# Optimization experiments

Hardware: AMD Instinct MI355X
Metric: run time of the kernel (lower is better)

## Reference

```python
import jax, jax.numpy as jnp
import numpy as np

B, N, RD = 32, 2000, 32
E, H, A = 128, 256, 8
NUM_ACTIONS = N
ACTION_NORM = float(NUM_ACTIONS)


def _mlp2(x, W1, b1, W2, b2):
    return jnp.maximum(x @ W1 + b1, 0.0) @ W2 + b2


def setup_inputs() -> dict:
    key = jax.random.key(0)
    ks = jax.random.split(key, 8)
    s = lambda fan_in: 1.0 / np.sqrt(fan_in)
    return {
        "state": jax.random.normal(ks[0], (B, N, RD), jnp.float32),
        "distance_matrix": jax.random.uniform(ks[1], (N, N), jnp.float32),
        "W_emb1": jax.random.normal(ks[2], (RD, H), jnp.float32) * s(RD),
        "b_emb1": jnp.zeros((H,), jnp.float32),
        "W_emb2": jax.random.normal(ks[3], (H, E), jnp.float32) * s(H),
        "b_emb2": jnp.zeros((E,), jnp.float32),
        "Wq1": jax.random.normal(ks[4], (E + A, H), jnp.float32) * s(E + A),
        "bq1": jnp.zeros((H,), jnp.float32),
        "Wq2": jax.random.normal(ks[5], (H, 1), jnp.float32) * s(H),
        "bq2": jnp.zeros((1,), jnp.float32),
        "fixed_actions": jax.random.randint(ks[6], (3, B), 0, NUM_ACTIONS, jnp.int32),
        "fixed_agent_ids": jnp.arange(3, dtype=jnp.int32),
    }


def reference(state, distance_matrix, W_emb1, b_emb1, W_emb2, b_emb2,
              Wq1, bq1, Wq2, bq2, fixed_actions, fixed_agent_ids):
    # normalized distance -> similarity, row-stochastic
    dm = distance_matrix / distance_matrix.max()
    sim = jnp.exp(-dm)  # scaling = 1 (use_nn_scaling=False)
    sim = sim / sim.sum(-1, keepdims=True)

    enc = _mlp2(state, W_emb1, b_emb1, W_emb2, b_emb2)      # [B,N,E]
    x = jnp.einsum('nm,bme->bne', sim, enc)                 # graph conv mix

    idx_f = jnp.arange(N, dtype=x.dtype)

    def qnet(actions):
        # actions: [B,A] broadcast over node axis -> concat -> MLP -> [B,N]
        act = jnp.broadcast_to(actions[:, None, :], (B, N, A))
        feat = jnp.concatenate([x, act], axis=-1)           # [B,N,E+A]
        return _mlp2(feat, Wq1, bq1, Wq2, bq2)[..., 0]      # [B,N]

    # init actions: -1 everywhere, fixed agents get given action / norm
    actions = jnp.full((B, A), -1.0, dtype=x.dtype)
    actions = actions.at[:, fixed_agent_ids].set(
        fixed_actions.T.astype(x.dtype) / ACTION_NORM)

    # sequential per-agent soft-argmax loop (second torch loop; the first
    # torch loop's q-values are fully overwritten here, so it is dead code)
    q_cols = []
    for agent_id in range(A):
        q = qnet(actions)                                   # [B,N]
        sam = jnp.clip(jax.nn.softmax(q, axis=-1) @ idx_f, 0.0, float(NUM_ACTIONS))
        actions = actions.at[:, agent_id].set(
            jax.lax.stop_gradient(sam / ACTION_NORM))
        q2 = qnet(actions)
        qv = jnp.take_along_axis(q2, sam.astype(jnp.int32)[:, None], axis=-1)[:, 0]
        q_cols.append(qv)

    q_values = jnp.stack(q_cols, axis=1)                    # [B,A]
    chosen = (actions * ACTION_NORM).astype(jnp.int32)      # [B,A]
    return q_values, chosen
```

## Files before the change

kernel.cpp:

```cpp
#include <hip/hip_runtime.h>
#include <cstddef>

#define NB 32
#define NN 2000
#define NRD 32
#define NE 128
#define NH 256
#define NA 8
#define KP8 2048
#define NGP 128
#define H1S 264
#define XT8S 136
#define ACTION_NORM 2000.0f

typedef unsigned short u16;
typedef unsigned char u8;
typedef __bf16 b16x8 __attribute__((ext_vector_type(8)));
typedef float f32x4 __attribute__((ext_vector_type(4)));
typedef const __attribute__((address_space(1))) unsigned int* gptr_t;
typedef __attribute__((address_space(3))) unsigned int* lptr_t;

__device__ inline u16 f2bf(float x) {
    unsigned u = __float_as_uint(x);
    u += 0x7FFFu + ((u >> 16) & 1u);
    return (u16)(u >> 16);
}
__device__ inline float bf2f(u16 h) { return __uint_as_float((unsigned)h << 16); }
__device__ inline u8 f2fp8(float x) {
    return (u8)(__builtin_amdgcn_cvt_pk_fp8_f32(x, x, 0, false) & 0xFF);
}
__device__ inline u16 f2fp8x2(float a, float b) {
    return (u16)(__builtin_amdgcn_cvt_pk_fp8_f32(a, b, 0, false) & 0xFFFF);
}
__device__ inline float fp82f(u8 b) {
    return __builtin_amdgcn_cvt_pk_f32_fp8((unsigned)b, false)[0];
}
__device__ inline int kswz(int m) {
    return (m & ~63) + (((m >> 3) & 3) << 4) + (((m >> 5) & 1) << 3) + (m & 7);
}

#define PREP_STATE (64000 * 32)
#define PREP_W1T   (256 * 32)
#define PREP_W2T   (128 * 256)
#define PREP_WQ1T  (256 * 128)
#define PREP_PAD   (4096 * 48)
#define PREP_TOT   (PREP_STATE + PREP_W1T + PREP_W2T + PREP_WQ1T + PREP_PAD)
#define PREP_BLOCKS (PREP_TOT / 256)
#define MAX_BLOCKS 1024
__global__ __launch_bounds__(256) void k_front(
        const float* __restrict__ state, const float* __restrict__ W1,
        const float* __restrict__ W2, const float* __restrict__ Wq1,
        const float* __restrict__ dm, const int* __restrict__ fa,
        const int* __restrict__ fid,
        u16* __restrict__ state_b, u16* __restrict__ W1t,
        u16* __restrict__ W2t, u8* __restrict__ Wq1f8,
        u8* __restrict__ encb, float* __restrict__ pmax,
        float* __restrict__ actions, float* __restrict__ ap0,
        float2* __restrict__ part0) {
    __shared__ float sh[256];
    const int blk = blockIdx.x, t = threadIdx.x;
    if (blk < PREP_BLOCKS) {
        int i = blk * 256 + t;
        if (i < PREP_STATE) { state_b[i] = f2bf(state[i]); return; }
        i -= PREP_STATE;
        if (i < PREP_W1T) { int h = i >> 5, k = i & 31; W1t[i] = f2bf(W1[k * NH + h]); return; }
        i -= PREP_W1T;
        if (i < PREP_W2T) { int e = i >> 8, h = i & 255; W2t[i] = f2bf(W2[h * NE + e]); return; }
        i -= PREP_W2T;
        if (i < PREP_WQ1T) { int hq = i >> 7, e = i & 127; Wq1f8[i] = f2fp8(Wq1[e * NH + hq]); return; }
        i -= PREP_WQ1T;
        if (i < PREP_PAD) { int eb = i / 48, mm = NN + (i % 48); encb[(size_t)eb * KP8 + kswz(mm)] = 0; }
        return;
    }
    if (blk < PREP_BLOCKS + MAX_BLOCKS) {
        const int bid = blk - PREP_BLOCKS;
        float m = 0.0f;
        for (size_t i = (size_t)bid * 256 + t; i < (size_t)NN * NN; i += (size_t)MAX_BLOCKS * 256)
            m = fmaxf(m, dm[i]);
        sh[t] = m; __syncthreads();
        for (int s = 128; s > 0; s >>= 1) {
            if (t < s) sh[t] = fmaxf(sh[t], sh[t + s]);
            __syncthreads();
        }
        if (t == 0) pmax[bid] = sh[0];
        return;
    }
    const int b = t >> 3, a = t & 7;
    float v = -1.0f;
    for (int j = 0; j < 3; ++j)
        if (fid[j] == a) v = (float)fa[j * NB + b] / ACTION_NORM;
    actions[t] = v;
    sh[t] = v;
    __syncthreads();
    float wq[NA];
#pragma unroll
    for (int aa = 0; aa < NA; ++aa) wq[aa] = Wq1[(size_t)(NE + aa) * NH + t];
    for (int bb = 0; bb < NB; ++bb) {
        float s = 0.0f;
#pragma unroll
        for (int aa = 0; aa < NA; ++aa) s = fmaf(sh[bb * NA + aa], wq[aa], s);
        ap0[bb * NH + t] = s;
    }
    for (int i = t; i < NB * NGP; i += 256) part0[i] = make_float2(0.0f, 0.0f);
}

__global__ __launch_bounds__(512) void k_sim_enc(
        const u16* __restrict__ state_b, const u16* __restrict__ W1t,
        const u16* __restrict__ W2t, u8* __restrict__ encb,
        const float* __restrict__ b1, const float* __restrict__ b2,
        const float* __restrict__ dm, const float* __restrict__ pmax,
        u8* __restrict__ simb, float* __restrict__ inv_rs) {
    __shared__ u16 stage[20 * 512];
    __shared__ u16 h1t[64 * H1S];
    const int blk = blockIdx.x, tid = threadIdx.x;

    if (blk >= 1000) {
        float* shf = (float*)stage;
        const int n = blk - 1000, t = tid;
        float m = fmaxf(pmax[t], pmax[t + 512]);
        shf[t] = m; __syncthreads();
        for (int s = 256; s > 0; s >>= 1) {
            if (t < s) shf[t] = fmaxf(shf[t], shf[t + s]);
            __syncthreads();
        }
        const float inv = 1.0f / shf[0];
        __syncthreads();
        float s = 0.0f;
        for (int mm = t * 2; mm < KP8; mm += 1024) {
            float e0 = 0.0f, e1 = 0.0f;
            if (mm < NN)     { e0 = expf(-dm[(size_t)n * NN + mm] * inv);     s += e0; }
            if (mm + 1 < NN) { e1 = expf(-dm[(size_t)n * NN + mm + 1] * inv); s += e1; }
            *(u16*)(simb + (size_t)n * KP8 + kswz(mm)) = f2fp8x2(e0, e1);
        }
        shf[t] = s; __syncthreads();
        for (int st = 256; st > 0; st >>= 1) {
            if (t < st) shf[t] += shf[t + st];
            __syncthreads();
        }
        if (t == 0) inv_rs[n] = 1.0f / shf[0];
        return;
    }

    const int w = tid >> 6, l = tid & 63;
    const int lm = l & 15, lq = l >> 4;
    const int gm = blk * 64;

    {
#pragma unroll
        for (int i = 0; i < 3; ++i) {
            const int idx = w * 3 + i;
            if (idx < 20) {
                const u16* gp;
                if (idx < 4) gp = state_b + (size_t)(gm + idx * 16 + lm) * NRD + lq * 8;
                else         gp = W1t + (size_t)((idx - 4) * 16 + lm) * NRD + lq * 8;
                __builtin_amdgcn_global_load_lds((gptr_t)gp, (lptr_t)(stage + idx * 512), 16, 0, 0);
            }
        }
        __syncthreads();
        b16x8 af[4], bf[2];
#pragma unroll
        for (int i = 0; i < 4; ++i) af[i] = *(const b16x8*)(stage + i * 512 + l * 8);
#pragma unroll
        for (int j = 0; j < 2; ++j) bf[j] = *(const b16x8*)(stage + (4 + w * 2 + j) * 512 + l * 8);
        f32x4 acc1[4][2] = {};
#pragma unroll
        for (int i = 0; i < 4; ++i)
#pragma unroll
            for (int j = 0; j < 2; ++j)
                acc1[i][j] = __builtin_amdgcn_mfma_f32_16x16x32_bf16(af[i], bf[j], acc1[i][j], 0, 0, 0);
#pragma unroll
        for (int i = 0; i < 4; ++i)
#pragma unroll
            for (int r = 0; r < 4; ++r) {
                const int row = i * 16 + lq * 4 + r;
#pragma unroll
                for (int j = 0; j < 2; ++j) {
                    const int col = w * 32 + j * 16 + lm;
                    h1t[row * H1S + col] = f2bf(fmaxf(acc1[i][j][r] + b1[col], 0.0f));
                }
            }
    }

    const int wr = w & 3, wc = w >> 2;
    f32x4 acc2[2][2] = {};
    const u16* gpw = W2t + (size_t)(w * 16 + lm) * NH + lq * 8;
    __syncthreads();
    __builtin_amdgcn_global_load_lds((gptr_t)gpw, (lptr_t)(stage + w * 512), 16, 0, 0);
    __syncthreads();
    for (int t = 0; t < 8; ++t) {
        const int cur = t & 1;
        if (t < 7) {
            gpw += 32;
            __builtin_amdgcn_global_load_lds((gptr_t)gpw,
                (lptr_t)(stage + (cur ^ 1) * 4096 + w * 512), 16, 0, 0);
        }
        const u16* base = stage + cur * 4096;
        b16x8 af2[2], bf2[2];
#pragma unroll
        for (int i = 0; i < 2; ++i)
            af2[i] = *(const b16x8*)(base + (wr * 2 + i) * 512 + l * 8);
#pragma unroll
        for (int j = 0; j < 2; ++j)
            bf2[j] = *(const b16x8*)(h1t + (wc * 32 + j * 16 + lm) * H1S + t * 32 + lq * 8);
#pragma unroll
        for (int i = 0; i < 2; ++i)
#pragma unroll
            for (int j = 0; j < 2; ++j)
                acc2[i][j] = __builtin_amdgcn_mfma_f32_16x16x32_bf16(af2[i], bf2[j], acc2[i][j], 0, 0, 0);
        __syncthreads();
    }
#pragma unroll
    for (int i = 0; i < 2; ++i)
#pragma unroll
        for (int r = 0; r < 4; ++r) {
            const int e = wr * 32 + i * 16 + lq * 4 + r;
            const float bias = b2[e];
#pragma unroll
            for (int j = 0; j < 2; ++j) {
                const int rg = gm + wc * 32 + j * 16 + lm;
                const unsigned bb = (unsigned)rg / 2000u;
                const unsigned mm = (unsigned)rg - bb * 2000u;
                encb[((size_t)bb * 128 + e) * KP8 + kswz((int)mm)] = f2fp8(acc2[i][j][r] + bias);
            }
        }
}

__global__ __launch_bounds__(512) void k_conv_y0(
        const u8* __restrict__ simb, const u8* __restrict__ encb,
        const u8* __restrict__ Wq1f8, const float* __restrict__ inv_rs,
        const float* __restrict__ bq1, const float* __restrict__ ap0,
        const float* __restrict__ Wq2, u8* __restrict__ y0f8,
        float2* __restrict__ part0) {
    __shared__ u8 lds[3 * 16384];
    __shared__ float qsum[64 * 8];
    const int tid = threadIdx.x;
    const int w = tid >> 6, l = tid & 63;
    const int wr = w & 1, wc = w >> 1;
    const int bm = blockIdx.x * 128;
    const int bb = blockIdx.y;
    const int lm = l & 15, lq = l >> 4;
    const u8* Bt = encb + (size_t)bb * 128 * KP8;
    typedef long lx2 __attribute__((ext_vector_type(2)));

    f32x4 acc[4][2] = {};

    const u8* gpt[2];
#pragma unroll
    for (int i = 0; i < 2; ++i) {
        const int idx = w * 2 + i;
        if (idx < 8) {
            int row = bm + idx * 16 + lm;
            row = row < NN ? row : NN - 1;
            gpt[i] = simb + (size_t)row * KP8 + lq * 16;
        } else {
            gpt[i] = Bt + (size_t)((idx - 8) * 16 + lm) * KP8 + lq * 16;
        }
    }

    auto STAGE = [&](int kt, int buf) {
#pragma unroll
        for (int i = 0; i < 2; ++i)
            __builtin_amdgcn_global_load_lds((gptr_t)(gpt[i] + kt * 64),
                (lptr_t)(lds + buf * 16384 + (w * 2 + i) * 1024), 16, 0, 0);
    };
    auto COMPUTE = [&](int buf) {
        const u8* curb = lds + buf * 16384;
        const int fo = l * 16;
        lx2 af[4], bf[2];
#pragma unroll
        for (int i = 0; i < 4; ++i)
            af[i] = *(const lx2*)(curb + (wr * 4 + i) * 1024 + fo);
#pragma unroll
        for (int j = 0; j < 2; ++j)
            bf[j] = *(const lx2*)(curb + (8 + wc * 2 + j) * 1024 + fo);
        __builtin_amdgcn_s_setprio(1);
#pragma unroll
        for (int i = 0; i < 4; ++i)
#pragma unroll
            for (int j = 0; j < 2; ++j) {
                acc[i][j] = __builtin_amdgcn_mfma_f32_16x16x32_fp8_fp8(af[i][0], bf[j][0], acc[i][j], 0, 0, 0);
                acc[i][j] = __builtin_amdgcn_mfma_f32_16x16x32_fp8_fp8(af[i][1], bf[j][1], acc[i][j], 0, 0, 0);
            }
        __builtin_amdgcn_s_setprio(0);
    };

#define FENCE() __builtin_amdgcn_sched_barrier(0)
#define BAR_BARE() do { FENCE(); asm volatile("" ::: "memory"); \
    __builtin_amdgcn_s_barrier(); FENCE(); } while (0)
#define BAR_VM(N) do { FENCE(); asm volatile("s_waitcnt vmcnt(" #N ")" ::: "memory"); \
    __builtin_amdgcn_s_barrier(); FENCE(); } while (0)

    STAGE(0, 0);
    STAGE(1, 1);
    for (int t = 0; t < 30; ++t) {
        STAGE(t + 2, (t + 2) % 3);
        BAR_VM(4);
        COMPUTE(t % 3);
        BAR_BARE();
    }
    BAR_VM(2);
    COMPUTE(0);
    BAR_BARE();
    BAR_VM(0);
    COMPUTE(1);
    BAR_BARE();
#undef BAR_VM
#undef BAR_BARE
#undef FENCE

#pragma unroll
    for (int i = 0; i < 4; ++i) {
#pragma unroll
        for (int r = 0; r < 4; ++r) {
            const int row = wr * 64 + i * 16 + lq * 4 + r;
            const int gn = bm + row;
            const float rsv = inv_rs[gn < NN ? gn : NN - 1];
#pragma unroll
            for (int j = 0; j < 2; ++j) {
                const int col = wc * 32 + j * 16 + lm;
                lds[row * XT8S + col] = f2fp8(acc[i][j][r] * rsv);
            }
        }
    }
    __syncthreads();

    const int h0 = w * 32;
    float bq1v[2], apv[2], w2vv[2];
#pragma unroll
    for (int j = 0; j < 2; ++j) {
        const int h = h0 + j * 16 + lm;
        bq1v[j] = bq1[h];
        apv[j] = ap0[bb * NH + h];
        w2vv[j] = Wq2[h];
    }
    float se_tot = 0.0f, sn_tot = 0.0f;

    for (int half = 0; half < 2; ++half) {
        f32x4 acc2[4][2] = {};
#pragma unroll
        for (int ks = 0; ks < 4; ++ks) {
            long bfw[2];
#pragma unroll
            for (int j = 0; j < 2; ++j)
                bfw[j] = *(const long*)(Wq1f8 + (size_t)(h0 + j * 16 + lm) * NE + ks * 32 + lq * 8);
#pragma unroll
            for (int i = 0; i < 4; ++i) {
                const long afx = *(const long*)(lds + (half * 64 + i * 16 + lm) * XT8S + ks * 32 + lq * 8);
#pragma unroll
                for (int j = 0; j < 2; ++j)
                    acc2[i][j] = __builtin_amdgcn_mfma_f32_16x16x32_fp8_fp8(afx, bfw[j], acc2[i][j], 0, 0, 0);
            }
        }
#pragma unroll
        for (int i = 0; i < 4; ++i) {
#pragma unroll
            for (int r = 0; r < 4; ++r) {
                const int rl = i * 16 + lq * 4 + r;
                const int n = bm + half * 64 + rl;
                float q = 0.0f;
#pragma unroll
                for (int j = 0; j < 2; ++j) {
                    const float v = acc2[i][j][r] + bq1v[j];
                    if (n < NN) y0f8[((size_t)n * NB + bb) * NH + h0 + j * 16 + lm] = f2fp8(v);
                    q += fmaxf(v + apv[j], 0.0f) * w2vv[j];
                }
#pragma unroll
                for (int off = 1; off < 16; off <<= 1) q += __shfl_xor(q, off);
                if (lm == 0) qsum[rl * 8 + w] = q;
            }
        }
        __syncthreads();
        if (tid < 64) {
            const int n = bm + half * 64 + tid;
            float q = 0.0f;
#pragma unroll
            for (int wv = 0; wv < 8; ++wv) q += qsum[tid * 8 + wv];
            float e = (n < NN) ? expf(fminf(q, 60.0f)) : 0.0f;
            float sne = e * (float)n;
#pragma unroll
            for (int off = 32; off > 0; off >>= 1) {
                e += __shfl_xor(e, off); sne += __shfl_xor(sne, off);
            }
            if (tid == 0) { se_tot += e; sn_tot += sne; }
        }
        __syncthreads();
    }
    if (tid == 0) part0[bb * NGP + blockIdx.x] = make_float2(se_tot, sn_tot);
}

__global__ __launch_bounds__(256) void k_agent(
        const u8* __restrict__ y0f8, const float* __restrict__ Wq1,
        const float* __restrict__ Wq2, const float* __restrict__ bq2,
        float* actions, const float2* __restrict__ pin, float2* __restrict__ pout,
        float* __restrict__ out, int ag) {
    __shared__ float sh[256];
    __shared__ float s_sam;
    const int t = threadIdx.x;
    const int lane = t & 63, wave = t >> 6;
    const int wg = blockIdx.x * 4 + wave;
    const int b = wg & 31, ng = wg >> 5;
    const int hl = lane & 15, qtr = lane >> 4;

    float act[NA];
#pragma unroll
    for (int a = 0; a < NA; ++a) act[a] = actions[b * NA + a];
    {
        const float2 p0 = pin[b * NGP + lane];
        const float2 p1 = pin[b * NGP + 64 + lane];
        float se0 = p0.x + p1.x, sn0 = p0.y + p1.y;
#pragma unroll
        for (int m = 32; m > 0; m >>= 1) {
            se0 += __shfl_xor(se0, m); sn0 += __shfl_xor(sn0, m);
        }
        const float sam = fminf(fmaxf(sn0 / se0, 0.0f), 2000.0f);
        act[ag - 1] = sam * (1.0f / ACTION_NORM);
    }
    float ap16[16] = {};
#pragma unroll
    for (int a = 0; a < NA; ++a) {
        const float av = act[a];
        const float4* wq = (const float4*)(Wq1 + (size_t)(NE + a) * NH + hl * 16);
#pragma unroll
        for (int jj = 0; jj < 4; ++jj) {
            const float4 w4 = wq[jj];
            ap16[jj * 4 + 0] = fmaf(av, w4.x, ap16[jj * 4 + 0]);
            ap16[jj * 4 + 1] = fmaf(av, w4.y, ap16[jj * 4 + 1]);
            ap16[jj * 4 + 2] = fmaf(av, w4.z, ap16[jj * 4 + 2]);
            ap16[jj * 4 + 3] = fmaf(av, w4.w, ap16[jj * 4 + 3]);
        }
    }
    float w2v[16];
    {
        const float4* w2p = (const float4*)(Wq2 + hl * 16);
#pragma unroll
        for (int jj = 0; jj < 4; ++jj) {
            const float4 w4 = w2p[jj];
            w2v[jj * 4 + 0] = w4.x; w2v[jj * 4 + 1] = w4.y;
            w2v[jj * 4 + 2] = w4.z; w2v[jj * 4 + 3] = w4.w;
        }
    }

    float se = 0.0f, sn = 0.0f;
#pragma unroll
    for (int k = 0; k < 4; ++k) {
        const int p = ng + k * NGP;
        if (p >= NN / 4) break;
        const int n = 4 * p + qtr;
        const uint4 yv = *(const uint4*)(y0f8 + (((size_t)n * NB + b) << 8) + hl * 16);
        const unsigned dw[4] = {yv.x, yv.y, yv.z, yv.w};
        float q = 0.0f;
#pragma unroll
        for (int d = 0; d < 4; ++d) {
            const auto lo = __builtin_amdgcn_cvt_pk_f32_fp8(dw[d], false);
            const auto hi = __builtin_amdgcn_cvt_pk_f32_fp8(dw[d], true);
            q += fmaxf(lo[0] + ap16[d * 4 + 0], 0.f) * w2v[d * 4 + 0];
            q += fmaxf(lo[1] + ap16[d * 4 + 1], 0.f) * w2v[d * 4 + 1];
            q += fmaxf(hi[0] + ap16[d * 4 + 2], 0.f) * w2v[d * 4 + 2];
            q += fmaxf(hi[1] + ap16[d * 4 + 3], 0.f) * w2v[d * 4 + 3];
        }
#pragma unroll
        for (int off = 1; off < 16; off <<= 1) q += __shfl_xor(q, off);
        const float e = expf(fminf(q, 60.0f));
        se += e; sn += e * (float)n;
    }
    se += __shfl_xor(se, 16); sn += __shfl_xor(sn, 16);
    se += __shfl_xor(se, 32); sn += __shfl_xor(sn, 32);
    if (lane == 0) pout[b * NGP + ng] = make_float2(se, sn);

    if (blockIdx.x < NB) {
        const int bb = blockIdx.x;
        if (wave == 0) {
            const float2 p0 = pin[bb * NGP + lane];
            const float2 p1 = pin[bb * NGP + 64 + lane];
            float a1 = p0.x + p1.x, a2 = p0.y + p1.y;
#pragma unroll
            for (int m = 32; m > 0; m >>= 1) {
                a1 += __shfl_xor(a1, m); a2 += __shfl_xor(a2, m);
            }
            if (lane == 0) s_sam = fminf(fmaxf(a2 / a1, 0.0f), 2000.0f);
        }
        __syncthreads();
        const float sam = s_sam;
        const float samn = sam * (1.0f / ACTION_NORM);
        float apt = 0.0f;
#pragma unroll
        for (int a = 0; a < NA; ++a) {
            const float av = (a == ag - 1) ? samn : actions[bb * NA + a];
            apt = fmaf(av, Wq1[(size_t)(NE + a) * NH + t], apt);
        }
        int nsel = (int)sam; if (nsel > NN - 1) nsel = NN - 1;
        const float yv = fp82f(y0f8[((size_t)nsel * NB + bb) * NH + t]);
        sh[t] = fmaxf(yv + apt, 0.0f) * Wq2[t];
        __syncthreads();
        for (int s = 128; s > 0; s >>= 1) {
            if (t < s) sh[t] += sh[t + s];
            __syncthreads();
        }
        if (t == 0) {
            out[bb * NA + (ag - 1)] = sh[0] + bq2[0];
            actions[bb * NA + (ag - 1)] = samn;
        }
    }
}

__global__ __launch_bounds__(256) void k_fin(
        const u8* __restrict__ y0f8, const float* __restrict__ Wq1,
        const float* __restrict__ Wq2, const float* __restrict__ bq2,
        const float* __restrict__ actions, const float2* __restrict__ pin,
        float* __restrict__ out) {
    __shared__ float sh[256];
    __shared__ float s_sam;
    const int bb = blockIdx.x, t = threadIdx.x;
    const int lane = t & 63, wave = t >> 6;
    if (wave == 0) {
        const float2 p0 = pin[bb * NGP + lane];
        const float2 p1 = pin[bb * NGP + 64 + lane];
        float a1 = p0.x + p1.x, a2 = p0.y + p1.y;
#pragma unroll
        for (int m = 32; m > 0; m >>= 1) {
            a1 += __shfl_xor(a1, m); a2 += __shfl_xor(a2, m);
        }
        if (lane == 0) s_sam = fminf(fmaxf(a2 / a1, 0.0f), 2000.0f);
    }
    __syncthreads();
    const float sam = s_sam;
    const float samn = sam * (1.0f / ACTION_NORM);
    float apt = 0.0f;
#pragma unroll
    for (int a = 0; a < NA; ++a) {
        const float av = (a == NA - 1) ? samn : actions[bb * NA + a];
        apt = fmaf(av, Wq1[(size_t)(NE + a) * NH + t], apt);
    }
    int nsel = (int)sam; if (nsel > NN - 1) nsel = NN - 1;
    const float yv = fp82f(y0f8[((size_t)nsel * NB + bb) * NH + t]);
    sh[t] = fmaxf(yv + apt, 0.0f) * Wq2[t];
    __syncthreads();
    for (int s = 128; s > 0; s >>= 1) {
        if (t < s) sh[t] += sh[t + s];
        __syncthreads();
    }
    if (t == 0) out[bb * NA + (NA - 1)] = sh[0] + bq2[0];
    if (t < NA) {
        const float av = (t == NA - 1) ? samn : actions[bb * NA + t];
        out[NB * NA + bb * NA + t] = (float)(int)(av * ACTION_NORM);
    }
}

extern "C" void kernel_launch(void* const* d_in, const int* in_sizes, int n_in,
                              void* d_out, int out_size, void* d_ws, size_t ws_size,
                              hipStream_t stream) {
    const float* state = (const float*)d_in[0];
    const float* dm    = (const float*)d_in[1];
    const float* W1    = (const float*)d_in[2];
    const float* b1    = (const float*)d_in[3];
    const float* W2    = (const float*)d_in[4];
    const float* b2    = (const float*)d_in[5];
    const float* Wq1   = (const float*)d_in[6];
    const float* bq1   = (const float*)d_in[7];
    const float* Wq2   = (const float*)d_in[8];
    const float* bq2   = (const float*)d_in[9];
    const int* fa      = (const int*)d_in[10];
    const int* fid     = (const int*)d_in[11];
    float* out = (float*)d_out;

    char* p = (char*)d_ws;
    u8* simb       = (u8*)p;       p += (size_t)NN * KP8;
    u8* encb       = (u8*)p;       p += (size_t)4096 * KP8;
    float* inv_rs  = (float*)p;    p += 2048 * 4;
    float* pmax    = (float*)p;    p += 1024 * 4;
    float* actions = (float*)p;    p += 256 * 4;
    float* ap0     = (float*)p;    p += 8192 * 4;
    float2* part0  = (float2*)p;   p += (size_t)NB * NGP * 8;
    float2* part1  = (float2*)p;   p += (size_t)NB * NGP * 8;
    u16* state_b   = (u16*)p;      p += (size_t)2048000 * 2;
    u16* W1t       = (u16*)p;      p += 8192 * 2;
    u16* W2t       = (u16*)p;      p += 32768 * 2;
    u8* Wq1f8      = (u8*)p;       p += 32768;
    u8* y0f8       = (u8*)p;       p += (size_t)16384000;

    k_front<<<PREP_BLOCKS + MAX_BLOCKS + 1, 256, 0, stream>>>(
        state, W1, W2, Wq1, dm, fa, fid,
        state_b, W1t, W2t, Wq1f8, encb, pmax, actions, ap0, part0);
    k_sim_enc<<<3000, 512, 0, stream>>>(state_b, W1t, W2t, encb, b1, b2,
                                        dm, pmax, simb, inv_rs);
    k_conv_y0<<<dim3(16, 32), 512, 0, stream>>>(simb, encb, Wq1f8, inv_rs, bq1,
                                                ap0, Wq2, y0f8, part0);
    for (int ag = 1; ag < NA; ++ag) {
        const float2* pin  = (ag & 1) ? part0 : part1;
        float2*       pout = (ag & 1) ? part1 : part0;
        k_agent<<<1024, 256, 0, stream>>>(y0f8, Wq1, Wq2, bq2, actions,
                                          pin, pout, out, ag);
    }
    k_fin<<<NB, 256, 0, stream>>>(y0f8, Wq1, Wq2, bq2, actions, part1, out);
}
```

Baseline: 260.0 us.

## Fuse sequential agent loop into one persistent per-batch kernel; deepen conv LDS ring

```diff
diff --git a/kernel.cpp b/kernel.cpp
--- a/kernel.cpp
+++ b/kernel.cpp
@@ -231,7 +231,7 @@
         const float* __restrict__ bq1, const float* __restrict__ ap0,
         const float* __restrict__ Wq2, u8* __restrict__ y0f8,
         float2* __restrict__ part0) {
-    __shared__ u8 lds[3 * 16384];
+    __shared__ u8 lds[4 * 16384];
     __shared__ float qsum[64 * 8];
     const int tid = threadIdx.x;
     const int w = tid >> 6, l = tid & 63;
@@ -285,27 +285,21 @@
     };
 
 #define FENCE() __builtin_amdgcn_sched_barrier(0)
-#define BAR_BARE() do { FENCE(); asm volatile("" ::: "memory"); \
-    __builtin_amdgcn_s_barrier(); FENCE(); } while (0)
 #define BAR_VM(N) do { FENCE(); asm volatile("s_waitcnt vmcnt(" #N ")" ::: "memory"); \
     __builtin_amdgcn_s_barrier(); FENCE(); } while (0)
 
     STAGE(0, 0);
     STAGE(1, 1);
     for (int t = 0; t < 30; ++t) {
-        STAGE(t + 2, (t + 2) % 3);
+        STAGE(t + 2, (t + 2) & 3);
         BAR_VM(4);
-        COMPUTE(t % 3);
-        BAR_BARE();
+        COMPUTE(t & 3);
     }
     BAR_VM(2);
-    COMPUTE(0);
-    BAR_BARE();
+    COMPUTE(2);
     BAR_VM(0);
-    COMPUTE(1);
-    BAR_BARE();
+    COMPUTE(3);
 #undef BAR_VM
-#undef BAR_BARE
 #undef FENCE
 
 #pragma unroll
@@ -388,161 +382,130 @@
     if (tid == 0) part0[bb * NGP + blockIdx.x] = make_float2(se_tot, sn_tot);
 }
 
-__global__ __launch_bounds__(256) void k_agent(
+__global__ __launch_bounds__(1024) void k_agents7(
         const u8* __restrict__ y0f8, const float* __restrict__ Wq1,
         const float* __restrict__ Wq2, const float* __restrict__ bq2,
-        float* actions, const float2* __restrict__ pin, float2* __restrict__ pout,
-        float* __restrict__ out, int ag) {
-    __shared__ float sh[256];
-    __shared__ float s_sam;
+        const float* __restrict__ actions, const float* __restrict__ ap0,
+        const float2* __restrict__ part0, float* __restrict__ out) {
+    __shared__ float s_w1r[NA][NH];
+    __shared__ float s_w2[NH];
+    __shared__ float2 s_part[16];
+    __shared__ float s_red[256];
+    const int b = blockIdx.x;
     const int t = threadIdx.x;
-    const int lane = t & 63, wave = t >> 6;
-    const int wg = blockIdx.x * 4 + wave;
-    const int b = wg & 31, ng = wg >> 5;
-    const int hl = lane & 15, qtr = lane >> 4;
+    const int l = t & 63, w = t >> 6;
+    const int hl = t & 15;
+    const int grp = t >> 4;
+
+    for (int i = t; i < NA * NH; i += 1024)
+        s_w1r[i >> 8][i & 255] = Wq1[(size_t)(NE + (i >> 8)) * NH + (i & 255)];
+    if (t < NH) s_w2[t] = Wq2[t];
 
     float act[NA];
 #pragma unroll
     for (int a = 0; a < NA; ++a) act[a] = actions[b * NA + a];
-    {
-        const float2 p0 = pin[b * NGP + lane];
-        const float2 p1 = pin[b * NGP + 64 + lane];
-        float se0 = p0.x + p1.x, sn0 = p0.y + p1.y;
-#pragma unroll
-        for (int m = 32; m > 0; m >>= 1) {
-            se0 += __shfl_xor(se0, m); sn0 += __shfl_xor(sn0, m);
-        }
-        const float sam = fminf(fmaxf(sn0 / se0, 0.0f), 2000.0f);
-        act[ag - 1] = sam * (1.0f / ACTION_NORM);
-    }
-    float ap16[16] = {};
-#pragma unroll
-    for (int a = 0; a < NA; ++a) {
-        const float av = act[a];
-        const float4* wq = (const float4*)(Wq1 + (size_t)(NE + a) * NH + hl * 16);
-#pragma unroll
-        for (int jj = 0; jj < 4; ++jj) {
-            const float4 w4 = wq[jj];
-            ap16[jj * 4 + 0] = fmaf(av, w4.x, ap16[jj * 4 + 0]);
-            ap16[jj * 4 + 1] = fmaf(av, w4.y, ap16[jj * 4 + 1]);
-            ap16[jj * 4 + 2] = fmaf(av, w4.z, ap16[jj * 4 + 2]);
-            ap16[jj * 4 + 3] = fmaf(av, w4.w, ap16[jj * 4 + 3]);
-        }
-    }
-    float w2v[16];
+    float w2v[16], ap16[16];
     {
         const float4* w2p = (const float4*)(Wq2 + hl * 16);
+        const float4* app = (const float4*)(ap0 + b * NH + hl * 16);
 #pragma unroll
         for (int jj = 0; jj < 4; ++jj) {
-            const float4 w4 = w2p[jj];
+            const float4 w4 = w2p[jj]; const float4 a4 = app[jj];
             w2v[jj * 4 + 0] = w4.x; w2v[jj * 4 + 1] = w4.y;
             w2v[jj * 4 + 2] = w4.z; w2v[jj * 4 + 3] = w4.w;
-        }
-    }
-
-    float se = 0.0f, sn = 0.0f;
-#pragma unroll
-    for (int k = 0; k < 4; ++k) {
-        const int p = ng + k * NGP;
-        if (p >= NN / 4) break;
-        const int n = 4 * p + qtr;
-        const uint4 yv = *(const uint4*)(y0f8 + (((size_t)n * NB + b) << 8) + hl * 16);
-        const unsigned dw[4] = {yv.x, yv.y, yv.z, yv.w};
-        float q = 0.0f;
-#pragma unroll
-        for (int d = 0; d < 4; ++d) {
-            const auto lo = __builtin_amdgcn_cvt_pk_f32_fp8(dw[d], false);
-            const auto hi = __builtin_amdgcn_cvt_pk_f32_fp8(dw[d], true);
-            q += fmaxf(lo[0] + ap16[d * 4 + 0], 0.f) * w2v[d * 4 + 0];
-            q += fmaxf(lo[1] + ap16[d * 4 + 1], 0.f) * w2v[d * 4 + 1];
-            q += fmaxf(hi[0] + ap16[d * 4 + 2], 0.f) * w2v[d * 4 + 2];
-            q += fmaxf(hi[1] + ap16[d * 4 + 3], 0.f) * w2v[d * 4 + 3];
-        }
-#pragma unroll
-        for (int off = 1; off < 16; off <<= 1) q += __shfl_xor(q, off);
-        const float e = expf(fminf(q, 60.0f));
-        se += e; sn += e * (float)n;
-    }
-    se += __shfl_xor(se, 16); sn += __shfl_xor(sn, 16);
-    se += __shfl_xor(se, 32); sn += __shfl_xor(sn, 32);
-    if (lane == 0) pout[b * NGP + ng] = make_float2(se, sn);
-
-    if (blockIdx.x < NB) {
-        const int bb = blockIdx.x;
-        if (wave == 0) {
-            const float2 p0 = pin[bb * NGP + lane];
-            const float2 p1 = pin[bb * NGP + 64 + lane];
-            float a1 = p0.x + p1.x, a2 = p0.y + p1.y;
+            ap16[jj * 4 + 0] = a4.x; ap16[jj * 4 + 1] = a4.y;
+            ap16[jj * 4 + 2] = a4.z; ap16[jj * 4 + 3] = a4.w;
+        }
+    }
+    __syncthreads();
+
+#pragma unroll
+    for (int ag = 1; ag <= NA; ++ag) {
+        const int idx = ag - 1;
+        float se0 = 0.0f, sn0 = 0.0f;
+        if (ag == 1) {
+            for (int s = l; s < NGP; s += 64) {
+                const float2 p = part0[b * NGP + s];
+                se0 += p.x; sn0 += p.y;
+            }
 #pragma unroll
             for (int m = 32; m > 0; m >>= 1) {
-                a1 += __shfl_xor(a1, m); a2 += __shfl_xor(a2, m);
-            }
-            if (lane == 0) s_sam = fminf(fmaxf(a2 / a1, 0.0f), 2000.0f);
-        }
-        __syncthreads();
-        const float sam = s_sam;
+                se0 += __shfl_xor(se0, m); sn0 += __shfl_xor(sn0, m);
+            }
+        } else {
+#pragma unroll
+            for (int s = 0; s < 16; ++s) {
+                const float2 p = s_part[s];
+                se0 += p.x; sn0 += p.y;
+            }
+        }
+        const float sam = fminf(fmaxf(sn0 / se0, 0.0f), 2000.0f);
         const float samn = sam * (1.0f / ACTION_NORM);
-        float apt = 0.0f;
-#pragma unroll
-        for (int a = 0; a < NA; ++a) {
-            const float av = (a == ag - 1) ? samn : actions[bb * NA + a];
-            apt = fmaf(av, Wq1[(size_t)(NE + a) * NH + t], apt);
-        }
+
+        const float d = samn - act[idx];
+        act[idx] = samn;
+#pragma unroll
+        for (int j = 0; j < 16; ++j)
+            ap16[j] = fmaf(d, s_w1r[idx][hl * 16 + j], ap16[j]);
+
         int nsel = (int)sam; if (nsel > NN - 1) nsel = NN - 1;
-        const float yv = fp82f(y0f8[((size_t)nsel * NB + bb) * NH + t]);
-        sh[t] = fmaxf(yv + apt, 0.0f) * Wq2[t];
-        __syncthreads();
-        for (int s = 128; s > 0; s >>= 1) {
-            if (t < s) sh[t] += sh[t + s];
+        __syncthreads();
+        if (t < NH) {
+            float apt = 0.0f;
+#pragma unroll
+            for (int a = 0; a < NA; ++a) apt = fmaf(act[a], s_w1r[a][t], apt);
+            const float yv = fp82f(y0f8[((size_t)nsel * NB + b) * NH + t]);
+            s_red[t] = fmaxf(yv + apt, 0.0f) * s_w2[t];
+        }
+        __syncthreads();
+        if (t < 128) s_red[t] += s_red[t + 128];
+        __syncthreads();
+        if (t < 64) {
+            float v = s_red[t] + s_red[t + 64];
+#pragma unroll
+            for (int m = 32; m > 0; m >>= 1) v += __shfl_xor(v, m);
+            if (t == 0) out[b * NA + idx] = v + bq2[0];
+        }
+
+        if (ag < NA) {
+            float se = 0.0f, sn = 0.0f;
+            for (int k = 0; k < 32; ++k) {
+                const int n = k * 64 + grp;
+                float q = 0.0f;
+                if (n < NN) {
+                    const uint4 yv = *(const uint4*)(y0f8 + ((size_t)n * NB + b) * NH + hl * 16);
+                    const unsigned dw[4] = {yv.x, yv.y, yv.z, yv.w};
+#pragma unroll
+                    for (int dd = 0; dd < 4; ++dd) {
+                        const auto lo = __builtin_amdgcn_cvt_pk_f32_fp8(dw[dd], false);
+                        const auto hi = __builtin_amdgcn_cvt_pk_f32_fp8(dw[dd], true);
+                        q += fmaxf(lo[0] + ap16[dd * 4 + 0], 0.f) * w2v[dd * 4 + 0];
+                        q += fmaxf(lo[1] + ap16[dd * 4 + 1], 0.f) * w2v[dd * 4 + 1];
+                        q += fmaxf(hi[0] + ap16[dd * 4 + 2], 0.f) * w2v[dd * 4 + 2];
+                        q += fmaxf(hi[1] + ap16[dd * 4 + 3], 0.f) * w2v[dd * 4 + 3];
+                    }
+                }
+#pragma unroll
+                for (int off = 1; off < 16; off <<= 1) q += __shfl_xor(q, off);
+                if (n < NN) {
+                    const float e = expf(fminf(q, 60.0f));
+                    se += e; sn += e * (float)n;
+                }
+            }
+            se += __shfl_xor(se, 16); sn += __shfl_xor(sn, 16);
+            se += __shfl_xor(se, 32); sn += __shfl_xor(sn, 32);
+            if (l == 0) s_part[w] = make_float2(se, sn);
             __syncthreads();
-        }
-        if (t == 0) {
-            out[bb * NA + (ag - 1)] = sh[0] + bq2[0];
-            actions[bb * NA + (ag - 1)] = samn;
-        }
-    }
-}
-
-__global__ __launch_bounds__(256) void k_fin(
-        const u8* __restrict__ y0f8, const float* __restrict__ Wq1,
-        const float* __restrict__ Wq2, const float* __restrict__ bq2,
-        const float* __restrict__ actions, const float2* __restrict__ pin,
-        float* __restrict__ out) {
-    __shared__ float sh[256];
-    __shared__ float s_sam;
-    const int bb = blockIdx.x, t = threadIdx.x;
-    const int lane = t & 63, wave = t >> 6;
-    if (wave == 0) {
-        const float2 p0 = pin[bb * NGP + lane];
-        const float2 p1 = pin[bb * NGP + 64 + lane];
-        float a1 = p0.x + p1.x, a2 = p0.y + p1.y;
-#pragma unroll
-        for (int m = 32; m > 0; m >>= 1) {
-            a1 += __shfl_xor(a1, m); a2 += __shfl_xor(a2, m);
-        }
-        if (lane == 0) s_sam = fminf(fmaxf(a2 / a1, 0.0f), 2000.0f);
-    }
-    __syncthreads();
-    const float sam = s_sam;
-    const float samn = sam * (1.0f / ACTION_NORM);
-    float apt = 0.0f;
-#pragma unroll
-    for (int a = 0; a < NA; ++a) {
-        const float av = (a == NA - 1) ? samn : actions[bb * NA + a];
-        apt = fmaf(av, Wq1[(size_t)(NE + a) * NH + t], apt);
-    }
-    int nsel = (int)sam; if (nsel > NN - 1) nsel = NN - 1;
-    const float yv = fp82f(y0f8[((size_t)nsel * NB + bb) * NH + t]);
-    sh[t] = fmaxf(yv + apt, 0.0f) * Wq2[t];
-    __syncthreads();
-    for (int s = 128; s > 0; s >>= 1) {
-        if (t < s) sh[t] += sh[t + s];
-        __syncthreads();
-    }
-    if (t == 0) out[bb * NA + (NA - 1)] = sh[0] + bq2[0];
-    if (t < NA) {
-        const float av = (t == NA - 1) ? samn : actions[bb * NA + t];
-        out[NB * NA + bb * NA + t] = (float)(int)(av * ACTION_NORM);
+        } else {
+            __syncthreads();
+            if (t == 0) {
+#pragma unroll
+                for (int a = 0; a < NA; ++a) s_red[a] = act[a];
+            }
+            __syncthreads();
+            if (t < NA)
+                out[NB * NA + b * NA + t] = (float)(int)(s_red[t] * ACTION_NORM);
+        }
     }
 }
 
@@ -585,11 +548,6 @@
                                         dm, pmax, simb, inv_rs);
     k_conv_y0<<<dim3(16, 32), 512, 0, stream>>>(simb, encb, Wq1f8, inv_rs, bq1,
                                                 ap0, Wq2, y0f8, part0);
-    for (int ag = 1; ag < NA; ++ag) {
-        const float2* pin  = (ag & 1) ? part0 : part1;
-        float2*       pout = (ag & 1) ? part1 : part0;
-        k_agent<<<1024, 256, 0, stream>>>(y0f8, Wq1, Wq2, bq2, actions,
-                                          pin, pout, out, ag);
-    }
-    k_fin<<<NB, 256, 0, stream>>>(y0f8, Wq1, Wq2, bq2, actions, part1, out);
-}
+    k_agents7<<<NB, 1024, 0, stream>>>(y0f8, Wq1, Wq2, bq2, actions, ap0,
+                                       part0, out);
+}
```

After: 338.6 us. 1.3x slower.
